# Kernel optimization log

Hardware: AMD Instinct MI355X
Metric: run time of the kernel (lower is better)

## Reference

```python
import jax, jax.numpy as jnp
import numpy as np

# ---- larq ste_sign: forward = sign (0 -> +1), backward = clipped straight-through ----
def _sign(x):
    return jnp.where(x >= 0, jnp.ones_like(x), -jnp.ones_like(x))

@jax.custom_vjp
def ste_sign(x):
    return _sign(x)

def _ste_fwd(x):
    return _sign(x), x

def _ste_bwd(x, g):
    return (g * (jnp.abs(x) <= 1.0).astype(g.dtype),)

ste_sign.defvjp(_ste_fwd, _ste_bwd)

BN_EPS = 1e-3  # keras BatchNormalization default epsilon

def conv2d(x, w, padding):
    # x: NHWC, w: HWIO
    return jax.lax.conv_general_dilated(
        x, w, window_strides=(1, 1), padding=padding,
        dimension_numbers=('NHWC', 'HWIO', 'NHWC'))

def maxpool2(x):
    return jax.lax.reduce_window(x, -jnp.inf, jax.lax.max,
                                 (1, 2, 2, 1), (1, 2, 2, 1), 'VALID')

def batchnorm(x, mean, var, beta):
    # BatchNormalization(scale=False): gamma fixed at 1
    return (x - mean) * jax.lax.rsqrt(var + BN_EPS) + beta


def setup_inputs() -> dict:
    key = jax.random.key(0)
    ks = jax.random.split(key, 20)
    d = {}
    d['x'] = jax.random.normal(ks[0], (64, 128, 128, 3), dtype=jnp.float32)
    d['w1'] = jax.random.normal(ks[1], (3, 3, 3, 32), dtype=jnp.float32)
    d['m1'] = jax.random.normal(ks[2], (32,), dtype=jnp.float32)
    d['v1'] = jax.random.uniform(ks[3], (32,), dtype=jnp.float32)
    d['b1'] = jax.random.normal(ks[4], (32,), dtype=jnp.float32)
    d['w2'] = jax.random.normal(ks[5], (3, 3, 32, 64), dtype=jnp.float32)
    d['m2'] = jax.random.normal(ks[6], (64,), dtype=jnp.float32)
    d['v2'] = jax.random.uniform(ks[7], (64,), dtype=jnp.float32)
    d['b2'] = jax.random.normal(ks[8], (64,), dtype=jnp.float32)
    d['w3'] = jax.random.normal(ks[9], (3, 3, 64, 128), dtype=jnp.float32)
    d['m3'] = jax.random.normal(ks[10], (128,), dtype=jnp.float32)
    d['v3'] = jax.random.uniform(ks[11], (128,), dtype=jnp.float32)
    d['b3'] = jax.random.normal(ks[12], (128,), dtype=jnp.float32)
    d['w4'] = jax.random.normal(ks[13], (3, 3, 128, 256), dtype=jnp.float32)
    d['m4'] = jax.random.normal(ks[14], (256,), dtype=jnp.float32)
    d['v4'] = jax.random.uniform(ks[15], (256,), dtype=jnp.float32)
    d['b4'] = jax.random.normal(ks[16], (256,), dtype=jnp.float32)
    return d


def reference(x, w1, m1, v1, b1, w2, m2, v2, b2, w3, m3, v3, b3, w4, m4, v4, b4):
    # Stem: QuantConv2D(32,3x3,valid) with kernel quantized only (no input quantizer)
    y = conv2d(x, ste_sign(w1), 'VALID')          # [B,126,126,32]
    y = batchnorm(maxpool2(y), m1, v1, b1)        # [B,63,63,32]
    # Three binarized blocks: ste_sign(input) conv ste_sign(kernel), same padding
    for w, m, v, b in ((w2, m2, v2, b2), (w3, m3, v3, b3), (w4, m4, v4, b4)):
        y = conv2d(ste_sign(y), ste_sign(w), 'SAME')
        y = batchnorm(maxpool2(y), m, v, b)       # halves spatial dims
    return y                                      # [B,7,7,256]
```

## Files before the change

kernel.cpp:

```cpp
#include <hip/hip_runtime.h>
#include <stdint.h>

#define BN_EPS 1e-3f

template <int CIN, int COUT>
__device__ inline void packw(const float* __restrict__ w, uint32_t* __restrict__ wp, int idx) {
    const int CINW = CIN / 32;
    int co = idx % COUT;
    int t2 = idx / COUT;
    int wi = t2 % CINW;
    int tap = t2 / CINW;
    uint32_t word = 0;
#pragma unroll
    for (int bb = 0; bb < 32; bb++) {
        float val = w[((tap * CIN) + wi * 32 + bb) * COUT + co];
        word |= (uint32_t)(val < 0.f) << bb;
    }
    wp[idx] = word;
}

__global__ void pack_all(const float* __restrict__ w1, const float* __restrict__ w2,
                         const float* __restrict__ w3, const float* __restrict__ w4,
                         float* __restrict__ w1s, uint32_t* __restrict__ w2p,
                         uint32_t* __restrict__ w3p, uint32_t* __restrict__ w4p) {
    int idx = blockIdx.x * 256 + threadIdx.x;
    if (idx < 864) {
        w1s[idx] = (w1[idx] < 0.f) ? -1.f : 1.f;
        return;
    }
    idx -= 864;
    if (idx < 576) { packw<32, 64>(w2, w2p, idx); return; }
    idx -= 576;
    if (idx < 2304) { packw<64, 128>(w3, w3p, idx); return; }
    idx -= 2304;
    if (idx < 9216) { packw<128, 256>(w4, w4p, idx); return; }
}

__global__ __launch_bounds__(256, 4) void conv1_k(const float* __restrict__ x,
                                                  const float* __restrict__ w1s,
                                                  const float* __restrict__ m1,
                                                  const float* __restrict__ v1,
                                                  const float* __restrict__ b1,
                                                  uint32_t* __restrict__ y1p) {
    __shared__ __align__(16) float xt[34 * 104];

    int tile = blockIdx.x;
    int tx = tile & 3;
    int ty = (tile >> 2) & 3;
    int n  = tile >> 4;
    int ph0 = ty * 16, pw0 = tx * 16;
    int r0 = 2 * ph0;
    int cf0 = pw0 * 6;

    for (int i = threadIdx.x; i < 34 * 102; i += 256) {
        int r = i / 102, c = i % 102;
        int gr = r0 + r, gcf = cf0 + c;
        float vv = 0.f;
        if (gr < 128 && gcf < 384)
            vv = x[(size_t)(n * 128 + gr) * 384 + gcf];
        xt[r * 104 + c] = vv;
    }

    __syncthreads();

    int wave = threadIdx.x >> 6, lane = threadIdx.x & 63;
    int px = lane & 15, py = (wave << 2) + (lane >> 4);
    int ph = ph0 + py, pw = pw0 + px;

    float win[48];
#pragma unroll
    for (int r = 0; r < 4; r++) {
        const float2* bp = (const float2*)&xt[(2 * py + r) * 104 + 6 * px];
#pragma unroll
        for (int q = 0; q < 6; q++) {
            float2 f2 = bp[q];
            win[r * 12 + 2 * q]     = f2.x;
            win[r * 12 + 2 * q + 1] = f2.y;
        }
    }

    uint32_t word = 0;
#pragma unroll 1
    for (int cg = 0; cg < 4; cg++) {
        float acc[8][4];
#pragma unroll
        for (int j = 0; j < 8; j++)
#pragma unroll
            for (int p = 0; p < 4; p++) acc[j][p] = 0.f;

        const float* sgc = w1s + cg * 8;
#pragma unroll
        for (int kh = 0; kh < 3; kh++)
#pragma unroll
            for (int kw = 0; kw < 3; kw++)
#pragma unroll
                for (int ci = 0; ci < 3; ci++) {
                    int tap = (kh * 3 + kw) * 3 + ci;
                    float x00 = win[kh * 12 + kw * 3 + ci];
                    float x01 = win[kh * 12 + (kw + 1) * 3 + ci];
                    float x10 = win[(kh + 1) * 12 + kw * 3 + ci];
                    float x11 = win[(kh + 1) * 12 + (kw + 1) * 3 + ci];
                    float4 s0 = *(const float4*)(sgc + tap * 32);
                    float4 s1 = *(const float4*)(sgc + tap * 32 + 4);
                    float sv[8] = {s0.x, s0.y, s0.z, s0.w, s1.x, s1.y, s1.z, s1.w};
#pragma unroll
                    for (int j = 0; j < 8; j++) {
                        acc[j][0] += x00 * sv[j];
                        acc[j][1] += x01 * sv[j];
                        acc[j][2] += x10 * sv[j];
                        acc[j][3] += x11 * sv[j];
                    }
                }
#pragma unroll
        for (int j = 0; j < 8; j++) {
            float mx = fmaxf(fmaxf(acc[j][0], acc[j][1]), fmaxf(acc[j][2], acc[j][3]));
            int ch = cg * 8 + j;
            float y = (mx - m1[ch]) * rsqrtf(v1[ch] + BN_EPS) + b1[ch];
            word |= (uint32_t)(y < 0.f) << ch;
        }
    }

    if (ph < 63 && pw < 63)
        y1p[(n * 63 + ph) * 63 + pw] = word;
}

__global__ __launch_bounds__(256) void bconv2(const uint32_t* __restrict__ y1p,
                                              const uint32_t* __restrict__ w2p,
                                              const float* __restrict__ m,
                                              const float* __restrict__ v,
                                              const float* __restrict__ b,
                                              uint2* __restrict__ y2p) {
    __shared__ uint32_t tile[4 * 64];

    int blk = blockIdx.x;
    int ph = blk % 31;
    int n  = blk / 31;
    int lane = threadIdx.x & 63;
    int wave = __builtin_amdgcn_readfirstlane(threadIdx.x >> 6);

    int row0 = 2 * ph - 1;
    for (int i = threadIdx.x; i < 4 * 63; i += 256) {
        int r = i / 63, c = i % 63;
        int rr = min(max(row0 + r, 0), 62);
        tile[r * 64 + c] = y1p[(n * 63 + rr) * 63 + c];
    }
    __syncthreads();

    uint32_t wq[9];
#pragma unroll
    for (int tap = 0; tap < 9; tap++) wq[tap] = w2p[tap * 64 + lane];
    float mm = m[lane], vv = v[lane], bb = b[lane];
    float rs = rsqrtf(vv + BN_EPS);

    for (int it = 0; it < 2; it++) {
        int pwg = wave * 2 + it;
        uint2 res[4];

        if (ph > 0 && pwg > 0) {
            int col0 = 8 * pwg - 1;
            uint32_t win[4][10];
#pragma unroll
            for (int r = 0; r < 4; r++)
#pragma unroll
                for (int c = 0; c < 10; c++)
                    win[r][c] = tile[r * 64 + min(col0 + c, 62)];

#pragma unroll
            for (int p = 0; p < 4; p++) {
                int a0 = 0, a1 = 0, a2 = 0, a3 = 0;
#pragma unroll
                for (int kh = 0; kh < 3; kh++)
#pragma unroll
                    for (int kw = 0; kw < 3; kw++) {
                        uint32_t w = wq[kh * 3 + kw];
                        a0 += __popc(win[kh][2 * p + kw] ^ w);
                        a1 += __popc(win[kh][2 * p + kw + 1] ^ w);
                        a2 += __popc(win[kh + 1][2 * p + kw] ^ w);
                        a3 += __popc(win[kh + 1][2 * p + kw + 1] ^ w);
                    }
                int mn = min(min(a0, a1), min(a2, a3));
                int best = 288 - 2 * mn;
                float y = ((float)best - mm) * rs + bb;
                unsigned long long bal = __ballot(y < 0.f);
                res[p] = make_uint2((uint32_t)bal, (uint32_t)(bal >> 32));
            }
        } else {
#pragma unroll
            for (int p = 0; p < 4; p++) {
                int pw = 4 * pwg + p;
                int best = -1000000;
                if (pw < 31) {
#pragma unroll
                    for (int dy = 0; dy < 2; dy++)
#pragma unroll
                        for (int dx = 0; dx < 2; dx++) {
                            int oh = 2 * ph + dy, ow = 2 * pw + dx;
                            int acc = 0, K = 0;
#pragma unroll
                            for (int kh = 0; kh < 3; kh++) {
                                int ih = oh - 1 + kh;
                                bool rok = (ih >= 0) && (ih < 63);
#pragma unroll
                                for (int kw = 0; kw < 3; kw++) {
                                    int iw = ow - 1 + kw;
                                    bool ok = rok && (iw >= 0) && (iw < 63);
                                    uint32_t wv = tile[(dy + kh) * 64 + min(max(iw, 0), 62)];
                                    if (ok) { acc += __popc(wv ^ wq[kh * 3 + kw]); K += 32; }
                                }
                            }
                            best = max(best, K - 2 * acc);
                        }
                }
                float y = ((float)best - mm) * rs + bb;
                unsigned long long bal = __ballot(y < 0.f);
                res[p] = make_uint2((uint32_t)bal, (uint32_t)(bal >> 32));
            }
        }

        uint2 rr = res[0];
        if (lane == 1) rr = res[1];
        if (lane == 2) rr = res[2];
        if (lane == 3) rr = res[3];
        int pws = 4 * pwg + lane;
        if (lane < 4 && pws < 31)
            y2p[(n * 31 + ph) * 31 + pws] = rr;
    }
}

__global__ __launch_bounds__(256) void bconv3(const uint2* __restrict__ y2p,
                                              const uint32_t* __restrict__ w3p,
                                              const float* __restrict__ m,
                                              const float* __restrict__ v,
                                              const float* __restrict__ b,
                                              uint32_t* __restrict__ y3p) {
    __shared__ uint2 tile[4 * 32];

    int blk = blockIdx.x;
    int ph = blk % 15;
    int n  = blk / 15;
    int lane = threadIdx.x & 63;
    int wave = __builtin_amdgcn_readfirstlane(threadIdx.x >> 6);
    int half = wave & 1;
    int co = half * 64 + lane;

    int row0 = 2 * ph - 1;
    for (int i = threadIdx.x; i < 4 * 31; i += 256) {
        int r = i / 31, c = i % 31;
        int rr = min(max(row0 + r, 0), 30);
        tile[r * 32 + c] = y2p[(n * 31 + rr) * 31 + c];
    }
    __syncthreads();

    uint32_t wq0[9], wq1[9];
#pragma unroll
    for (int tap = 0; tap < 9; tap++) {
        wq0[tap] = w3p[(tap * 2 + 0) * 128 + co];
        wq1[tap] = w3p[(tap * 2 + 1) * 128 + co];
    }
    float mm = m[co], vv = v[co], bb = b[co];
    float rs = rsqrtf(vv + BN_EPS);

    for (int it = 0; it < 4; it++) {
        int pwg = (wave >> 1) * 4 + it;
        unsigned long long bal0, bal1;

        if (ph > 0 && pwg > 0) {
            int col0 = 4 * pwg - 1;
            uint2 win[4][6];
#pragma unroll
            for (int r = 0; r < 4; r++)
#pragma unroll
                for (int c = 0; c < 6; c++)
                    win[r][c] = tile[r * 32 + min(col0 + c, 30)];

            unsigned long long bals[2];
#pragma unroll
            for (int p = 0; p < 2; p++) {
                int a0 = 0, a1 = 0, a2 = 0, a3 = 0;
#pragma unroll
                for (int kh = 0; kh < 3; kh++)
#pragma unroll
                    for (int kw = 0; kw < 3; kw++) {
                        int tap = kh * 3 + kw;
                        uint32_t u0 = wq0[tap], u1 = wq1[tap];
                        a0 += __popc(win[kh][2 * p + kw].x ^ u0) + __popc(win[kh][2 * p + kw].y ^ u1);
                        a1 += __popc(win[kh][2 * p + kw + 1].x ^ u0) + __popc(win[kh][2 * p + kw + 1].y ^ u1);
                        a2 += __popc(win[kh + 1][2 * p + kw].x ^ u0) + __popc(win[kh + 1][2 * p + kw].y ^ u1);
                        a3 += __popc(win[kh + 1][2 * p + kw + 1].x ^ u0) + __popc(win[kh + 1][2 * p + kw + 1].y ^ u1);
                    }
                int mn = min(min(a0, a1), min(a2, a3));
                int best = 576 - 2 * mn;
                float y = ((float)best - mm) * rs + bb;
                bals[p] = __ballot(y < 0.f);
            }
            bal0 = bals[0]; bal1 = bals[1];
        } else {
            unsigned long long bals[2];
#pragma unroll
            for (int p = 0; p < 2; p++) {
                int pw = 2 * pwg + p;
                int best = -1000000;
                if (pw < 15) {
#pragma unroll
                    for (int dy = 0; dy < 2; dy++)
#pragma unroll
                        for (int dx = 0; dx < 2; dx++) {
                            int oh = 2 * ph + dy, ow = 2 * pw + dx;
                            int acc = 0, K = 0;
#pragma unroll
                            for (int kh = 0; kh < 3; kh++) {
                                int ih = oh - 1 + kh;
                                bool rok = (ih >= 0) && (ih < 31);
#pragma unroll
                                for (int kw = 0; kw < 3; kw++) {
                                    int iw = ow - 1 + kw;
                                    bool ok = rok && (iw >= 0) && (iw < 31);
                                    uint2 iv = tile[(dy + kh) * 32 + min(max(iw, 0), 30)];
                                    int tap = kh * 3 + kw;
                                    if (ok) {
                                        acc += __popc(iv.x ^ wq0[tap]) + __popc(iv.y ^ wq1[tap]);
                                        K += 64;
                                    }
                                }
                            }
                            best = max(best, K - 2 * acc);
                        }
                }
                float y = ((float)best - mm) * rs + bb;
                bals[p] = __ballot(y < 0.f);
            }
            bal0 = bals[0]; bal1 = bals[1];
        }

        uint32_t val = (uint32_t)bal0;
        if (lane == 1) val = (uint32_t)(bal0 >> 32);
        if (lane == 2) val = (uint32_t)bal1;
        if (lane == 3) val = (uint32_t)(bal1 >> 32);
        int p = lane >> 1;
        int pw = 2 * pwg + p;
        if (lane < 4 && pw < 15) {
            int pixel = (n * 15 + ph) * 15 + pw;
            y3p[pixel * 4 + half * 2 + (lane & 1)] = val;
        }
    }
}

__global__ __launch_bounds__(256) void bconv4(const uint4* __restrict__ y3p,
                                              const uint32_t* __restrict__ w4p,
                                              const float* __restrict__ m,
                                              const float* __restrict__ v,
                                              const float* __restrict__ b,
                                              float* __restrict__ out) {
    __shared__ __align__(16) uint32_t tile[64];

    int pixel = blockIdx.x;
    int lane = threadIdx.x & 63;
    int co = (threadIdx.x >> 6) * 64 + lane;
    int pw = pixel % 7;
    int t = pixel / 7;
    int ph = t % 7;
    int n = t / 7;

    if (threadIdx.x < 64) {
        int tt = threadIdx.x;
        int r = tt >> 4, e = (tt >> 2) & 3, w = tt & 3;
        int gr = 2 * ph - 1 + r, gc = 2 * pw - 1 + e;
        uint32_t val = 0;
        if (gr >= 0 && gr < 15 && gc >= 0 && gc < 15)
            val = ((const uint32_t*)y3p)[(((size_t)(n * 15 + gr) * 15 + gc) << 2) + w];
        tile[tt] = val;
    }
    __syncthreads();

    const uint4* tp = (const uint4*)tile;

    uint4 wq[9];
#pragma unroll
    for (int tap = 0; tap < 9; tap++) {
        wq[tap].x = w4p[(tap * 4 + 0) * 256 + co];
        wq[tap].y = w4p[(tap * 4 + 1) * 256 + co];
        wq[tap].z = w4p[(tap * 4 + 2) * 256 + co];
        wq[tap].w = w4p[(tap * 4 + 3) * 256 + co];
    }

    int best;
    if (ph > 0 && pw > 0) {
        int a0 = 0, a1 = 0, a2 = 0, a3 = 0;
#pragma unroll
        for (int r = 0; r < 4; r++)
#pragma unroll
            for (int c = 0; c < 4; c++) {
                uint4 iv = tp[r * 4 + c];
#pragma unroll
                for (int kh = 0; kh < 3; kh++) {
                    int dy = r - kh;
                    if (dy < 0 || dy > 1) continue;
#pragma unroll
                    for (int kw = 0; kw < 3; kw++) {
                        int dx = c - kw;
                        if (dx < 0 || dx > 1) continue;
                        int tap = kh * 3 + kw;
                        int pc = __popc(iv.x ^ wq[tap].x) + __popc(iv.y ^ wq[tap].y)
                               + __popc(iv.z ^ wq[tap].z) + __popc(iv.w ^ wq[tap].w);
                        if (dy == 0 && dx == 0) a0 += pc;
                        else if (dy == 0) a1 += pc;
                        else if (dx == 0) a2 += pc;
                        else a3 += pc;
                    }
                }
            }
        best = max(max(1152 - 2 * a0, 1152 - 2 * a1), max(1152 - 2 * a2, 1152 - 2 * a3));
    } else {
        best = -1000000;
#pragma unroll
        for (int dy = 0; dy < 2; dy++)
#pragma unroll
            for (int dx = 0; dx < 2; dx++) {
                int oh = 2 * ph + dy, ow = 2 * pw + dx;
                int acc = 0, K = 0;
#pragma unroll
                for (int kh = 0; kh < 3; kh++) {
                    int ih = oh - 1 + kh;
                    if (ih < 0 || ih >= 15) continue;
#pragma unroll
                    for (int kw = 0; kw < 3; kw++) {
                        int iw = ow - 1 + kw;
                        if (iw < 0 || iw >= 15) continue;
                        uint4 iv = tp[(dy + kh) * 4 + (dx + kw)];
                        int tap = kh * 3 + kw;
                        acc += __popc(iv.x ^ wq[tap].x) + __popc(iv.y ^ wq[tap].y)
                             + __popc(iv.z ^ wq[tap].z) + __popc(iv.w ^ wq[tap].w);
                        K += 128;
                    }
                }
                best = max(best, K - 2 * acc);
            }
    }
    float y = ((float)best - m[co]) * rsqrtf(v[co] + BN_EPS) + b[co];
    out[pixel * 256 + co] = y;
}

extern "C" void kernel_launch(void* const* d_in, const int* in_sizes, int n_in,
                              void* d_out, int out_size, void* d_ws, size_t ws_size,
                              hipStream_t stream) {
    const float* x  = (const float*)d_in[0];
    const float* w1 = (const float*)d_in[1];
    const float* m1 = (const float*)d_in[2];
    const float* v1 = (const float*)d_in[3];
    const float* b1 = (const float*)d_in[4];
    const float* w2 = (const float*)d_in[5];
    const float* m2 = (const float*)d_in[6];
    const float* v2 = (const float*)d_in[7];
    const float* b2 = (const float*)d_in[8];
    const float* w3 = (const float*)d_in[9];
    const float* m3 = (const float*)d_in[10];
    const float* v3 = (const float*)d_in[11];
    const float* b3 = (const float*)d_in[12];
    const float* w4 = (const float*)d_in[13];
    const float* m4 = (const float*)d_in[14];
    const float* v4 = (const float*)d_in[15];
    const float* b4 = (const float*)d_in[16];
    float* out = (float*)d_out;

    char* ws = (char*)d_ws;
    size_t off = 0;
    auto take = [&](size_t bytes) -> char* {
        char* p = ws + off;
        off += (bytes + 255) & ~(size_t)255;
        return p;
    };
    uint32_t* y1p = (uint32_t*)take((size_t)64 * 63 * 63 * 4);
    uint2*    y2p = (uint2*)take((size_t)64 * 31 * 31 * 8);
    uint32_t* y3p = (uint32_t*)take((size_t)64 * 15 * 15 * 16);
    float*    w1s = (float*)take(864 * 4);
    uint32_t* w2p = (uint32_t*)take(576 * 4);
    uint32_t* w3p = (uint32_t*)take(2304 * 4);
    uint32_t* w4p = (uint32_t*)take(9216 * 4);

    pack_all<<<(864 + 576 + 2304 + 9216 + 255) / 256, 256, 0, stream>>>(
        w1, w2, w3, w4, w1s, w2p, w3p, w4p);

    conv1_k<<<64 * 16, 256, 0, stream>>>(x, w1s, m1, v1, b1, y1p);

    bconv2<<<64 * 31, 256, 0, stream>>>(y1p, w2p, m2, v2, b2, y2p);

    bconv3<<<64 * 15, 256, 0, stream>>>(y2p, w3p, m3, v3, b3, y3p);

    bconv4<<<64 * 7 * 7, 256, 0, stream>>>((const uint4*)y3p, w4p, m4, v4, b4, out);
}
```

Baseline: 207.3 us.

## Stage conv1 weights and BN params in LDS, widen channel groups

```diff
diff --git a/kernel.cpp b/kernel.cpp
--- a/kernel.cpp
+++ b/kernel.cpp
@@ -36,13 +36,15 @@
     if (idx < 9216) { packw<128, 256>(w4, w4p, idx); return; }
 }
 
-__global__ __launch_bounds__(256, 4) void conv1_k(const float* __restrict__ x,
+__global__ __launch_bounds__(256, 2) void conv1_k(const float* __restrict__ x,
                                                   const float* __restrict__ w1s,
                                                   const float* __restrict__ m1,
                                                   const float* __restrict__ v1,
                                                   const float* __restrict__ b1,
                                                   uint32_t* __restrict__ y1p) {
     __shared__ __align__(16) float xt[34 * 104];
+    __shared__ __align__(16) float wsh[864];
+    __shared__ float bnsh[96];
 
     int tile = blockIdx.x;
     int tx = tile & 3;
@@ -60,6 +62,13 @@
             vv = x[(size_t)(n * 128 + gr) * 384 + gcf];
         xt[r * 104 + c] = vv;
     }
+    for (int i = threadIdx.x; i < 864; i += 256)
+        wsh[i] = w1s[i];
+    if (threadIdx.x < 96) {
+        int t = threadIdx.x;
+        float v = (t < 32) ? m1[t] : (t < 64) ? v1[t - 32] : b1[t - 64];
+        bnsh[t] = v;
+    }
 
     __syncthreads();
 
@@ -67,28 +76,17 @@
     int px = lane & 15, py = (wave << 2) + (lane >> 4);
     int ph = ph0 + py, pw = pw0 + px;
 
-    float win[48];
-#pragma unroll
-    for (int r = 0; r < 4; r++) {
-        const float2* bp = (const float2*)&xt[(2 * py + r) * 104 + 6 * px];
-#pragma unroll
-        for (int q = 0; q < 6; q++) {
-            float2 f2 = bp[q];
-            win[r * 12 + 2 * q]     = f2.x;
-            win[r * 12 + 2 * q + 1] = f2.y;
-        }
-    }
+    const float* xb = &xt[(2 * py) * 104 + 6 * px];
 
     uint32_t word = 0;
 #pragma unroll 1
-    for (int cg = 0; cg < 4; cg++) {
-        float acc[8][4];
-#pragma unroll
-        for (int j = 0; j < 8; j++)
+    for (int cg = 0; cg < 2; cg++) {
+        float acc[16][4];
+#pragma unroll
+        for (int j = 0; j < 16; j++)
 #pragma unroll
             for (int p = 0; p < 4; p++) acc[j][p] = 0.f;
 
-        const float* sgc = w1s + cg * 8;
 #pragma unroll
         for (int kh = 0; kh < 3; kh++)
 #pragma unroll
@@ -96,26 +94,29 @@
 #pragma unroll
                 for (int ci = 0; ci < 3; ci++) {
                     int tap = (kh * 3 + kw) * 3 + ci;
-                    float x00 = win[kh * 12 + kw * 3 + ci];
-                    float x01 = win[kh * 12 + (kw + 1) * 3 + ci];
-                    float x10 = win[(kh + 1) * 12 + kw * 3 + ci];
-                    float x11 = win[(kh + 1) * 12 + (kw + 1) * 3 + ci];
-                    float4 s0 = *(const float4*)(sgc + tap * 32);
-                    float4 s1 = *(const float4*)(sgc + tap * 32 + 4);
-                    float sv[8] = {s0.x, s0.y, s0.z, s0.w, s1.x, s1.y, s1.z, s1.w};
-#pragma unroll
-                    for (int j = 0; j < 8; j++) {
-                        acc[j][0] += x00 * sv[j];
-                        acc[j][1] += x01 * sv[j];
-                        acc[j][2] += x10 * sv[j];
-                        acc[j][3] += x11 * sv[j];
-                    }
+                    const float* xp = xb + kh * 104 + kw * 3 + ci;
+                    float x00 = xp[0];
+                    float x01 = xp[3];
+                    float x10 = xp[104];
+                    float x11 = xp[107];
+                    const float4* wvp = (const float4*)(wsh + tap * 32 + cg * 16);
+                    float4 wA = wvp[0], wB = wvp[1], wC = wvp[2], wD = wvp[3];
+#define FMA4(WV, C0)                                                           \
+    { float w_ = (WV);                                                         \
+      acc[C0][0] += x00 * w_; acc[C0][1] += x01 * w_;                          \
+      acc[C0][2] += x10 * w_; acc[C0][3] += x11 * w_; }
+                    FMA4(wA.x, 0)  FMA4(wA.y, 1)  FMA4(wA.z, 2)  FMA4(wA.w, 3)
+                    FMA4(wB.x, 4)  FMA4(wB.y, 5)  FMA4(wB.z, 6)  FMA4(wB.w, 7)
+                    FMA4(wC.x, 8)  FMA4(wC.y, 9)  FMA4(wC.z, 10) FMA4(wC.w, 11)
+                    FMA4(wD.x, 12) FMA4(wD.y, 13) FMA4(wD.z, 14) FMA4(wD.w, 15)
+#undef FMA4
                 }
-#pragma unroll
-        for (int j = 0; j < 8; j++) {
+
+#pragma unroll
+        for (int j = 0; j < 16; j++) {
             float mx = fmaxf(fmaxf(acc[j][0], acc[j][1]), fmaxf(acc[j][2], acc[j][3]));
-            int ch = cg * 8 + j;
-            float y = (mx - m1[ch]) * rsqrtf(v1[ch] + BN_EPS) + b1[ch];
+            int ch = cg * 16 + j;
+            float y = (mx - bnsh[ch]) * rsqrtf(bnsh[32 + ch] + BN_EPS) + bnsh[64 + ch];
             word |= (uint32_t)(y < 0.f) << ch;
         }
     }
@@ -124,12 +125,12 @@
         y1p[(n * 63 + ph) * 63 + pw] = word;
 }
 
-__global__ __launch_bounds__(256) void bconv2(const uint32_t* __restrict__ y1p,
-                                              const uint32_t* __restrict__ w2p,
-                                              const float* __restrict__ m,
-                                              const float* __restrict__ v,
-                                              const float* __restrict__ b,
-                                              uint2* __restrict__ y2p) {
+__global__ __launch_bounds__(256, 2) void bconv2(const uint32_t* __restrict__ y1p,
+                                                 const uint32_t* __restrict__ w2p,
+                                                 const float* __restrict__ m,
+                                                 const float* __restrict__ v,
+                                                 const float* __restrict__ b,
+                                                 uint2* __restrict__ y2p) {
     __shared__ uint32_t tile[4 * 64];
 
     int blk = blockIdx.x;
@@ -227,12 +228,12 @@
     }
 }
 
-__global__ __launch_bounds__(256) void bconv3(const uint2* __restrict__ y2p,
-                                              const uint32_t* __restrict__ w3p,
-                                              const float* __restrict__ m,
-                                              const float* __restrict__ v,
-                                              const float* __restrict__ b,
-                                              uint32_t* __restrict__ y3p) {
+__global__ __launch_bounds__(256, 2) void bconv3(const uint2* __restrict__ y2p,
+                                                 const uint32_t* __restrict__ w3p,
+                                                 const float* __restrict__ m,
+                                                 const float* __restrict__ v,
+                                                 const float* __restrict__ b,
+                                                 uint32_t* __restrict__ y3p) {
     __shared__ uint2 tile[4 * 32];
 
     int blk = blockIdx.x;
@@ -345,12 +346,12 @@
     }
 }
 
-__global__ __launch_bounds__(256) void bconv4(const uint4* __restrict__ y3p,
-                                              const uint32_t* __restrict__ w4p,
-                                              const float* __restrict__ m,
-                                              const float* __restrict__ v,
-                                              const float* __restrict__ b,
-                                              float* __restrict__ out) {
+__global__ __launch_bounds__(256, 2) void bconv4(const uint4* __restrict__ y3p,
+                                                 const uint32_t* __restrict__ w4p,
+                                                 const float* __restrict__ m,
+                                                 const float* __restrict__ v,
+                                                 const float* __restrict__ b,
+                                                 float* __restrict__ out) {
     __shared__ __align__(16) uint32_t tile[64];
 
     int pixel = blockIdx.x;
```

Result: no change. 206.3 us (-0.5%).

## Fuse all stages into one persistent cooperative kernel with grid syncs

Applied to the files above, without the earlier changes.

```diff
diff --git a/kernel.cpp b/kernel.cpp
--- a/kernel.cpp
+++ b/kernel.cpp
@@ -1,5 +1,8 @@
 #include <hip/hip_runtime.h>
+#include <hip/hip_cooperative_groups.h>
 #include <stdint.h>
+
+namespace cg = cooperative_groups;
 
 #define BN_EPS 1e-3f
 
@@ -19,6 +22,439 @@
     wp[idx] = word;
 }
 
+struct FusedParams {
+    const float *x, *w1, *m1, *v1, *b1;
+    const float *w2, *m2, *v2, *b2;
+    const float *w3, *m3, *v3, *b3;
+    const float *w4, *m4, *v4, *b4;
+    float* out;
+    uint32_t* y1p;
+    uint2* y2p;
+    uint32_t* y3p;
+    float* w1s;
+    uint32_t *w2p, *w3p, *w4p;
+};
+
+__global__ __launch_bounds__(256, 4) void fused_all(FusedParams P) {
+    __shared__ __align__(16) float smem[34 * 104];
+    cg::grid_group grid = cg::this_grid();
+    const int tid = threadIdx.x;
+    const int nblk = gridDim.x;
+
+    {
+        int idx = blockIdx.x * 256 + tid;
+        if (idx < 864) {
+            P.w1s[idx] = (P.w1[idx] < 0.f) ? -1.f : 1.f;
+        } else {
+            idx -= 864;
+            if (idx < 576) { packw<32, 64>(P.w2, P.w2p, idx); }
+            else {
+                idx -= 576;
+                if (idx < 2304) { packw<64, 128>(P.w3, P.w3p, idx); }
+                else {
+                    idx -= 2304;
+                    if (idx < 9216) { packw<128, 256>(P.w4, P.w4p, idx); }
+                }
+            }
+        }
+    }
+    grid.sync();
+
+    {
+        int wave = tid >> 6, lane = tid & 63;
+        int px = lane & 15, py = (wave << 2) + (lane >> 4);
+        for (int tile = blockIdx.x; tile < 1024; tile += nblk) {
+            int tx = tile & 3;
+            int ty = (tile >> 2) & 3;
+            int n  = tile >> 4;
+            int ph0 = ty * 16, pw0 = tx * 16;
+            int r0 = 2 * ph0;
+            int cf0 = pw0 * 6;
+
+            for (int i = tid; i < 34 * 102; i += 256) {
+                int r = i / 102, c = i % 102;
+                int gr = r0 + r, gcf = cf0 + c;
+                float vv = 0.f;
+                if (gr < 128 && gcf < 384)
+                    vv = P.x[(size_t)(n * 128 + gr) * 384 + gcf];
+                smem[r * 104 + c] = vv;
+            }
+            __syncthreads();
+
+            int ph = ph0 + py, pw = pw0 + px;
+
+            float win[48];
+#pragma unroll
+            for (int r = 0; r < 4; r++) {
+                const float2* bp = (const float2*)&smem[(2 * py + r) * 104 + 6 * px];
+#pragma unroll
+                for (int q = 0; q < 6; q++) {
+                    float2 f2 = bp[q];
+                    win[r * 12 + 2 * q]     = f2.x;
+                    win[r * 12 + 2 * q + 1] = f2.y;
+                }
+            }
+
+            uint32_t word = 0;
+#pragma unroll 1
+            for (int g = 0; g < 4; g++) {
+                float acc[8][4];
+#pragma unroll
+                for (int j = 0; j < 8; j++)
+#pragma unroll
+                    for (int p = 0; p < 4; p++) acc[j][p] = 0.f;
+
+                const float* sgc = P.w1s + g * 8;
+#pragma unroll
+                for (int kh = 0; kh < 3; kh++)
+#pragma unroll
+                    for (int kw = 0; kw < 3; kw++)
+#pragma unroll
+                        for (int ci = 0; ci < 3; ci++) {
+                            int tap = (kh * 3 + kw) * 3 + ci;
+                            float x00 = win[kh * 12 + kw * 3 + ci];
+                            float x01 = win[kh * 12 + (kw + 1) * 3 + ci];
+                            float x10 = win[(kh + 1) * 12 + kw * 3 + ci];
+                            float x11 = win[(kh + 1) * 12 + (kw + 1) * 3 + ci];
+                            float4 s0 = *(const float4*)(sgc + tap * 32);
+                            float4 s1 = *(const float4*)(sgc + tap * 32 + 4);
+                            float sv[8] = {s0.x, s0.y, s0.z, s0.w, s1.x, s1.y, s1.z, s1.w};
+#pragma unroll
+                            for (int j = 0; j < 8; j++) {
+                                acc[j][0] += x00 * sv[j];
+                                acc[j][1] += x01 * sv[j];
+                                acc[j][2] += x10 * sv[j];
+                                acc[j][3] += x11 * sv[j];
+                            }
+                        }
+#pragma unroll
+                for (int j = 0; j < 8; j++) {
+                    float mx = fmaxf(fmaxf(acc[j][0], acc[j][1]), fmaxf(acc[j][2], acc[j][3]));
+                    int ch = g * 8 + j;
+                    float y = (mx - P.m1[ch]) * rsqrtf(P.v1[ch] + BN_EPS) + P.b1[ch];
+                    word |= (uint32_t)(y < 0.f) << ch;
+                }
+            }
+
+            if (ph < 63 && pw < 63)
+                P.y1p[(n * 63 + ph) * 63 + pw] = word;
+            __syncthreads();
+        }
+    }
+    grid.sync();
+
+    {
+        uint32_t* tl = (uint32_t*)smem;
+        int lane = tid & 63;
+        int wave = __builtin_amdgcn_readfirstlane(tid >> 6);
+
+        uint32_t wq[9];
+#pragma unroll
+        for (int tap = 0; tap < 9; tap++) wq[tap] = P.w2p[tap * 64 + lane];
+        float mm = P.m2[lane];
+        float rs = rsqrtf(P.v2[lane] + BN_EPS);
+        float bb = P.b2[lane];
+
+        for (int blk = blockIdx.x; blk < 64 * 31; blk += nblk) {
+            int ph = blk % 31;
+            int n  = blk / 31;
+            int row0 = 2 * ph - 1;
+            for (int i = tid; i < 4 * 63; i += 256) {
+                int r = i / 63, c = i % 63;
+                int rr = min(max(row0 + r, 0), 62);
+                tl[r * 64 + c] = P.y1p[(n * 63 + rr) * 63 + c];
+            }
+            __syncthreads();
+
+            for (int it = 0; it < 2; it++) {
+                int pwg = wave * 2 + it;
+                uint2 res[4];
+
+                if (ph > 0 && pwg > 0) {
+                    int col0 = 8 * pwg - 1;
+                    uint32_t win[4][10];
+#pragma unroll
+                    for (int r = 0; r < 4; r++)
+#pragma unroll
+                        for (int c = 0; c < 10; c++)
+                            win[r][c] = tl[r * 64 + min(col0 + c, 62)];
+
+#pragma unroll
+                    for (int p = 0; p < 4; p++) {
+                        int a0 = 0, a1 = 0, a2 = 0, a3 = 0;
+#pragma unroll
+                        for (int kh = 0; kh < 3; kh++)
+#pragma unroll
+                            for (int kw = 0; kw < 3; kw++) {
+                                uint32_t w = wq[kh * 3 + kw];
+                                a0 += __popc(win[kh][2 * p + kw] ^ w);
+                                a1 += __popc(win[kh][2 * p + kw + 1] ^ w);
+                                a2 += __popc(win[kh + 1][2 * p + kw] ^ w);
+                                a3 += __popc(win[kh + 1][2 * p + kw + 1] ^ w);
+                            }
+                        int mn = min(min(a0, a1), min(a2, a3));
+                        int best = 288 - 2 * mn;
+                        float y = ((float)best - mm) * rs + bb;
+                        unsigned long long bal = __ballot(y < 0.f);
+                        res[p] = make_uint2((uint32_t)bal, (uint32_t)(bal >> 32));
+                    }
+                } else {
+#pragma unroll
+                    for (int p = 0; p < 4; p++) {
+                        int pw = 4 * pwg + p;
+                        int best = -1000000;
+                        if (pw < 31) {
+#pragma unroll
+                            for (int dy = 0; dy < 2; dy++)
+#pragma unroll
+                                for (int dx = 0; dx < 2; dx++) {
+                                    int oh = 2 * ph + dy, ow = 2 * pw + dx;
+                                    int acc = 0, K = 0;
+#pragma unroll
+                                    for (int kh = 0; kh < 3; kh++) {
+                                        int ih = oh - 1 + kh;
+                                        bool rok = (ih >= 0) && (ih < 63);
+#pragma unroll
+                                        for (int kw = 0; kw < 3; kw++) {
+                                            int iw = ow - 1 + kw;
+                                            bool ok = rok && (iw >= 0) && (iw < 63);
+                                            uint32_t wv = tl[(dy + kh) * 64 + min(max(iw, 0), 62)];
+                                            if (ok) { acc += __popc(wv ^ wq[kh * 3 + kw]); K += 32; }
+                                        }
+                                    }
+                                    best = max(best, K - 2 * acc);
+                                }
+                        }
+                        float y = ((float)best - mm) * rs + bb;
+                        unsigned long long bal = __ballot(y < 0.f);
+                        res[p] = make_uint2((uint32_t)bal, (uint32_t)(bal >> 32));
+                    }
+                }
+
+                uint2 rr = res[0];
+                if (lane == 1) rr = res[1];
+                if (lane == 2) rr = res[2];
+                if (lane == 3) rr = res[3];
+                int pws = 4 * pwg + lane;
+                if (lane < 4 && pws < 31)
+                    P.y2p[(n * 31 + ph) * 31 + pws] = rr;
+            }
+            __syncthreads();
+        }
+    }
+    grid.sync();
+
+    {
+        uint2* tl = (uint2*)smem;
+        int lane = tid & 63;
+        int wave = __builtin_amdgcn_readfirstlane(tid >> 6);
+        int half = wave & 1;
+        int co = half * 64 + lane;
+
+        uint32_t wq0[9], wq1[9];
+#pragma unroll
+        for (int tap = 0; tap < 9; tap++) {
+            wq0[tap] = P.w3p[(tap * 2 + 0) * 128 + co];
+            wq1[tap] = P.w3p[(tap * 2 + 1) * 128 + co];
+        }
+        float mm = P.m3[co];
+        float rs = rsqrtf(P.v3[co] + BN_EPS);
+        float bb = P.b3[co];
+
+        for (int blk = blockIdx.x; blk < 64 * 15; blk += nblk) {
+            int ph = blk % 15;
+            int n  = blk / 15;
+            int row0 = 2 * ph - 1;
+            for (int i = tid; i < 4 * 31; i += 256) {
+                int r = i / 31, c = i % 31;
+                int rr = min(max(row0 + r, 0), 30);
+                tl[r * 32 + c] = P.y2p[(n * 31 + rr) * 31 + c];
+            }
+            __syncthreads();
+
+            for (int it = 0; it < 4; it++) {
+                int pwg = (wave >> 1) * 4 + it;
+                unsigned long long bal0, bal1;
+
+                if (ph > 0 && pwg > 0) {
+                    int col0 = 4 * pwg - 1;
+                    uint2 win[4][6];
+#pragma unroll
+                    for (int r = 0; r < 4; r++)
+#pragma unroll
+                        for (int c = 0; c < 6; c++)
+                            win[r][c] = tl[r * 32 + min(col0 + c, 30)];
+
+                    unsigned long long bals[2];
+#pragma unroll
+                    for (int p = 0; p < 2; p++) {
+                        int a0 = 0, a1 = 0, a2 = 0, a3 = 0;
+#pragma unroll
+                        for (int kh = 0; kh < 3; kh++)
+#pragma unroll
+                            for (int kw = 0; kw < 3; kw++) {
+                                int tap = kh * 3 + kw;
+                                uint32_t u0 = wq0[tap], u1 = wq1[tap];
+                                a0 += __popc(win[kh][2 * p + kw].x ^ u0) + __popc(win[kh][2 * p + kw].y ^ u1);
+                                a1 += __popc(win[kh][2 * p + kw + 1].x ^ u0) + __popc(win[kh][2 * p + kw + 1].y ^ u1);
+                                a2 += __popc(win[kh + 1][2 * p + kw].x ^ u0) + __popc(win[kh + 1][2 * p + kw].y ^ u1);
+                                a3 += __popc(win[kh + 1][2 * p + kw + 1].x ^ u0) + __popc(win[kh + 1][2 * p + kw + 1].y ^ u1);
+                            }
+                        int mn = min(min(a0, a1), min(a2, a3));
+                        int best = 576 - 2 * mn;
+                        float y = ((float)best - mm) * rs + bb;
+                        bals[p] = __ballot(y < 0.f);
+                    }
+                    bal0 = bals[0]; bal1 = bals[1];
+                } else {
+                    unsigned long long bals[2];
+#pragma unroll
+                    for (int p = 0; p < 2; p++) {
+                        int pw = 2 * pwg + p;
+                        int best = -1000000;
+                        if (pw < 15) {
+#pragma unroll
+                            for (int dy = 0; dy < 2; dy++)
+#pragma unroll
+                                for (int dx = 0; dx < 2; dx++) {
+                                    int oh = 2 * ph + dy, ow = 2 * pw + dx;
+                                    int acc = 0, K = 0;
+#pragma unroll
+                                    for (int kh = 0; kh < 3; kh++) {
+                                        int ih = oh - 1 + kh;
+                                        bool rok = (ih >= 0) && (ih < 31);
+#pragma unroll
+                                        for (int kw = 0; kw < 3; kw++) {
+                                            int iw = ow - 1 + kw;
+                                            bool ok = rok && (iw >= 0) && (iw < 31);
+                                            uint2 iv = tl[(dy + kh) * 32 + min(max(iw, 0), 30)];
+                                            int tap = kh * 3 + kw;
+                                            if (ok) {
+                                                acc += __popc(iv.x ^ wq0[tap]) + __popc(iv.y ^ wq1[tap]);
+                                                K += 64;
+                                            }
+                                        }
+                                    }
+                                    best = max(best, K - 2 * acc);
+                                }
+                        }
+                        float y = ((float)best - mm) * rs + bb;
+                        bals[p] = __ballot(y < 0.f);
+                    }
+                    bal0 = bals[0]; bal1 = bals[1];
+                }
+
+                uint32_t val = (uint32_t)bal0;
+                if (lane == 1) val = (uint32_t)(bal0 >> 32);
+                if (lane == 2) val = (uint32_t)bal1;
+                if (lane == 3) val = (uint32_t)(bal1 >> 32);
+                int p = lane >> 1;
+                int pw = 2 * pwg + p;
+                if (lane < 4 && pw < 15) {
+                    int pixel = (n * 15 + ph) * 15 + pw;
+                    P.y3p[pixel * 4 + half * 2 + (lane & 1)] = val;
+                }
+            }
+            __syncthreads();
+        }
+    }
+    grid.sync();
+
+    {
+        uint32_t* tl = (uint32_t*)smem;
+        const uint4* tp = (const uint4*)tl;
+        int lane = tid & 63;
+        int co = (tid >> 6) * 64 + lane;
+
+        uint4 wq[9];
+#pragma unroll
+        for (int tap = 0; tap < 9; tap++) {
+            wq[tap].x = P.w4p[(tap * 4 + 0) * 256 + co];
+            wq[tap].y = P.w4p[(tap * 4 + 1) * 256 + co];
+            wq[tap].z = P.w4p[(tap * 4 + 2) * 256 + co];
+            wq[tap].w = P.w4p[(tap * 4 + 3) * 256 + co];
+        }
+        float mm = P.m4[co];
+        float rs = rsqrtf(P.v4[co] + BN_EPS);
+        float bbv = P.b4[co];
+
+        for (int pixel = blockIdx.x; pixel < 64 * 7 * 7; pixel += nblk) {
+            int pw = pixel % 7;
+            int t = pixel / 7;
+            int ph = t % 7;
+            int n = t / 7;
+
+            if (tid < 64) {
+                int tt = tid;
+                int r = tt >> 4, e = (tt >> 2) & 3, w = tt & 3;
+                int gr = 2 * ph - 1 + r, gc = 2 * pw - 1 + e;
+                uint32_t val = 0;
+                if (gr >= 0 && gr < 15 && gc >= 0 && gc < 15)
+                    val = P.y3p[(((size_t)(n * 15 + gr) * 15 + gc) << 2) + w];
+                tl[tt] = val;
+            }
+            __syncthreads();
+
+            int best;
+            if (ph > 0 && pw > 0) {
+                int a0 = 0, a1 = 0, a2 = 0, a3 = 0;
+#pragma unroll
+                for (int r = 0; r < 4; r++)
+#pragma unroll
+                    for (int c = 0; c < 4; c++) {
+                        uint4 iv = tp[r * 4 + c];
+#pragma unroll
+                        for (int kh = 0; kh < 3; kh++) {
+                            int dy = r - kh;
+                            if (dy < 0 || dy > 1) continue;
+#pragma unroll
+                            for (int kw = 0; kw < 3; kw++) {
+                                int dx = c - kw;
+                                if (dx < 0 || dx > 1) continue;
+                                int tap = kh * 3 + kw;
+                                int pc = __popc(iv.x ^ wq[tap].x) + __popc(iv.y ^ wq[tap].y)
+                                       + __popc(iv.z ^ wq[tap].z) + __popc(iv.w ^ wq[tap].w);
+                                if (dy == 0 && dx == 0) a0 += pc;
+                                else if (dy == 0) a1 += pc;
+                                else if (dx == 0) a2 += pc;
+                                else a3 += pc;
+                            }
+                        }
+                    }
+                best = max(max(1152 - 2 * a0, 1152 - 2 * a1), max(1152 - 2 * a2, 1152 - 2 * a3));
+            } else {
+                best = -1000000;
+#pragma unroll
+                for (int dy = 0; dy < 2; dy++)
+#pragma unroll
+                    for (int dx = 0; dx < 2; dx++) {
+                        int oh = 2 * ph + dy, ow = 2 * pw + dx;
+                        int acc = 0, K = 0;
+#pragma unroll
+                        for (int kh = 0; kh < 3; kh++) {
+                            int ih = oh - 1 + kh;
+                            if (ih < 0 || ih >= 15) continue;
+#pragma unroll
+                            for (int kw = 0; kw < 3; kw++) {
+                                int iw = ow - 1 + kw;
+                                if (iw < 0 || iw >= 15) continue;
+                                uint4 iv = tp[(dy + kh) * 4 + (dx + kw)];
+                                int tap = kh * 3 + kw;
+                                acc += __popc(iv.x ^ wq[tap].x) + __popc(iv.y ^ wq[tap].y)
+                                     + __popc(iv.z ^ wq[tap].z) + __popc(iv.w ^ wq[tap].w);
+                                K += 128;
+                            }
+                        }
+                        best = max(best, K - 2 * acc);
+                    }
+            }
+            float y = ((float)best - mm) * rs + bbv;
+            P.out[pixel * 256 + co] = y;
+            __syncthreads();
+        }
+    }
+}
+
 __global__ void pack_all(const float* __restrict__ w1, const float* __restrict__ w2,
                          const float* __restrict__ w3, const float* __restrict__ w4,
                          float* __restrict__ w1s, uint32_t* __restrict__ w2p,
@@ -60,7 +496,6 @@
             vv = x[(size_t)(n * 128 + gr) * 384 + gcf];
         xt[r * 104 + c] = vv;
     }
-
     __syncthreads();
 
     int wave = threadIdx.x >> 6, lane = threadIdx.x & 63;
@@ -81,14 +516,14 @@
 
     uint32_t word = 0;
 #pragma unroll 1
-    for (int cg = 0; cg < 4; cg++) {
+    for (int g = 0; g < 4; g++) {
         float acc[8][4];
 #pragma unroll
         for (int j = 0; j < 8; j++)
 #pragma unroll
             for (int p = 0; p < 4; p++) acc[j][p] = 0.f;
 
-        const float* sgc = w1s + cg * 8;
+        const float* sgc = w1s + g * 8;
 #pragma unroll
         for (int kh = 0; kh < 3; kh++)
 #pragma unroll
@@ -114,7 +549,7 @@
 #pragma unroll
         for (int j = 0; j < 8; j++) {
             float mx = fmaxf(fmaxf(acc[j][0], acc[j][1]), fmaxf(acc[j][2], acc[j][3]));
-            int ch = cg * 8 + j;
+            int ch = g * 8 + j;
             float y = (mx - m1[ch]) * rsqrtf(v1[ch] + BN_EPS) + b1[ch];
             word |= (uint32_t)(y < 0.f) << ch;
         }
@@ -124,12 +559,12 @@
         y1p[(n * 63 + ph) * 63 + pw] = word;
 }
 
-__global__ __launch_bounds__(256) void bconv2(const uint32_t* __restrict__ y1p,
-                                              const uint32_t* __restrict__ w2p,
-                                              const float* __restrict__ m,
-                                              const float* __restrict__ v,
-                                              const float* __restrict__ b,
-                                              uint2* __restrict__ y2p) {
+__global__ __launch_bounds__(256, 2) void bconv2(const uint32_t* __restrict__ y1p,
+                                                 const uint32_t* __restrict__ w2p,
+                                                 const float* __restrict__ m,
+                                                 const float* __restrict__ v,
+                                                 const float* __restrict__ b,
+                                                 uint2* __restrict__ y2p) {
     __shared__ uint32_t tile[4 * 64];
 
     int blk = blockIdx.x;
@@ -227,12 +662,12 @@
     }
 }
 
-__global__ __launch_bounds__(256) void bconv3(const uint2* __restrict__ y2p,
-                                              const uint32_t* __restrict__ w3p,
-                                              const float* __restrict__ m,
-                                              const float* __restrict__ v,
-                                              const float* __restrict__ b,
-                                              uint32_t* __restrict__ y3p) {
+__global__ __launch_bounds__(256, 2) void bconv3(const uint2* __restrict__ y2p,
+                                                 const uint32_t* __restrict__ w3p,
+                                                 const float* __restrict__ m,
+                                                 const float* __restrict__ v,
+                                                 const float* __restrict__ b,
+                                                 uint32_t* __restrict__ y3p) {
     __shared__ uint2 tile[4 * 32];
 
     int blk = blockIdx.x;
@@ -345,12 +780,12 @@
     }
 }
 
-__global__ __launch_bounds__(256) void bconv4(const uint4* __restrict__ y3p,
-                                              const uint32_t* __restrict__ w4p,
-                                              const float* __restrict__ m,
-                                              const float* __restrict__ v,
-                                              const float* __restrict__ b,
-                                              float* __restrict__ out) {
+__global__ __launch_bounds__(256, 2) void bconv4(const uint4* __restrict__ y3p,
+                                                 const uint32_t* __restrict__ w4p,
+                                                 const float* __restrict__ m,
+                                                 const float* __restrict__ v,
+                                                 const float* __restrict__ b,
+                                                 float* __restrict__ out) {
     __shared__ __align__(16) uint32_t tile[64];
 
     int pixel = blockIdx.x;
@@ -477,14 +912,35 @@
     uint32_t* w3p = (uint32_t*)take(2304 * 4);
     uint32_t* w4p = (uint32_t*)take(9216 * 4);
 
-    pack_all<<<(864 + 576 + 2304 + 9216 + 255) / 256, 256, 0, stream>>>(
-        w1, w2, w3, w4, w1s, w2p, w3p, w4p);
-
-    conv1_k<<<64 * 16, 256, 0, stream>>>(x, w1s, m1, v1, b1, y1p);
-
-    bconv2<<<64 * 31, 256, 0, stream>>>(y1p, w2p, m2, v2, b2, y2p);
-
-    bconv3<<<64 * 15, 256, 0, stream>>>(y2p, w3p, m3, v3, b3, y3p);
-
-    bconv4<<<64 * 7 * 7, 256, 0, stream>>>((const uint4*)y3p, w4p, m4, v4, b4, out);
+    FusedParams P;
+    P.x = x; P.w1 = w1; P.m1 = m1; P.v1 = v1; P.b1 = b1;
+    P.w2 = w2; P.m2 = m2; P.v2 = v2; P.b2 = b2;
+    P.w3 = w3; P.m3 = m3; P.v3 = v3; P.b3 = b3;
+    P.w4 = w4; P.m4 = m4; P.v4 = v4; P.b4 = b4;
+    P.out = out;
+    P.y1p = y1p; P.y2p = y2p; P.y3p = y3p;
+    P.w1s = w1s; P.w2p = w2p; P.w3p = w3p; P.w4p = w4p;
+
+    bool launched = false;
+    int perMP = 0;
+    hipError_t qe = hipOccupancyMaxActiveBlocksPerMultiprocessor(
+        &perMP, (const void*)fused_all, 256, 0);
+    if (qe == hipSuccess && perMP >= 1) {
+        int gridn = perMP * 256;
+        if (gridn > 1024) gridn = 1024;
+        void* args[] = { (void*)&P };
+        hipError_t le = hipLaunchCooperativeKernel((const void*)fused_all,
+                                                   dim3(gridn), dim3(256),
+                                                   args, 0, stream);
+        launched = (le == hipSuccess);
+    }
+
+    if (!launched) {
+        pack_all<<<(864 + 576 + 2304 + 9216 + 255) / 256, 256, 0, stream>>>(
+            w1, w2, w3, w4, w1s, w2p, w3p, w4p);
+        conv1_k<<<64 * 16, 256, 0, stream>>>(x, w1s, m1, v1, b1, y1p);
+        bconv2<<<64 * 31, 256, 0, stream>>>(y1p, w2p, m2, v2, b2, y2p);
+        bconv3<<<64 * 15, 256, 0, stream>>>(y2p, w3p, m3, v3, b3, y3p);
+        bconv4<<<64 * 7 * 7, 256, 0, stream>>>((const uint4*)y3p, w4p, m4, v4, b4, out);
+    }
 }
```

Result: slower. 451.1 us (+117.6%).
